# Optimization experiments

Measured on AMD Instinct MI355X. Metric: run time of the kernel, lower is better.

Reference implementation:

```python
import jax, jax.numpy as jnp
import numpy as np

T = 200                      # TRAIN_ROIS_PER_IMAGE
RATIO = 0.33                 # ROI_POSITIVE_RATIO
P_MAX = int(T * RATIO)       # max positive ROIs (66)
MH, MW = 28, 28              # MASK_SHAPE
STD = jnp.array([0.1, 0.1, 0.2, 0.2], jnp.float32)  # BBOX_STD_DEV
EPS = 1e-6


def _iou(a, b):
    # a [N,4], b [G,4] -> [N,G] IoU (same math as overlaps_graph, without tiling)
    ay1, ax1, ay2, ax2 = a[:, 0:1], a[:, 1:2], a[:, 2:3], a[:, 3:4]
    by1, bx1, by2, bx2 = b[None, :, 0], b[None, :, 1], b[None, :, 2], b[None, :, 3]
    iy = jnp.maximum(jnp.minimum(ay2, by2) - jnp.maximum(ay1, by1), 0.0)
    ix = jnp.maximum(jnp.minimum(ax2, bx2) - jnp.maximum(ax1, bx1), 0.0)
    inter = iy * ix
    union = (ay2 - ay1) * (ax2 - ax1) + (by2 - by1) * (bx2 - bx1) - inter
    return inter / jnp.maximum(union, EPS)


def _box_refinement(box, gt):
    # standard Mask R-CNN box_refinement_graph
    h = jnp.maximum(box[:, 2] - box[:, 0], EPS)
    w = jnp.maximum(box[:, 3] - box[:, 1], EPS)
    cy = box[:, 0] + 0.5 * h
    cx = box[:, 1] + 0.5 * w
    gh = jnp.maximum(gt[:, 2] - gt[:, 0], EPS)
    gw = jnp.maximum(gt[:, 3] - gt[:, 1], EPS)
    gcy = gt[:, 0] + 0.5 * gh
    gcx = gt[:, 1] + 0.5 * gw
    return jnp.stack([(gcy - cy) / h, (gcx - cx) / w,
                      jnp.log(gh / h), jnp.log(gw / w)], axis=-1)


def _crop_and_resize(imgs, boxes):
    # imgs [T,H,W], boxes [T,4] normalized; TF crop_and_resize bilinear semantics,
    # extrapolation_value = 0 for samples outside [0, H-1] x [0, W-1].
    Tn, H, W = imgs.shape
    y1, x1, y2, x2 = boxes[:, 0], boxes[:, 1], boxes[:, 2], boxes[:, 3]
    iy = jnp.arange(MH, dtype=jnp.float32)
    ix = jnp.arange(MW, dtype=jnp.float32)
    ys = y1[:, None] * (H - 1) + iy[None, :] * ((y2 - y1) * (H - 1) / (MH - 1))[:, None]  # [T,MH]
    xs = x1[:, None] * (W - 1) + ix[None, :] * ((x2 - x1) * (W - 1) / (MW - 1))[:, None]  # [T,MW]
    y0 = jnp.floor(ys); x0 = jnp.floor(xs)
    wy = (ys - y0)[:, :, None]
    wx = (xs - x0)[:, None, :]
    y0i = jnp.clip(y0, 0, H - 1).astype(jnp.int32)
    y1i = jnp.clip(y0 + 1, 0, H - 1).astype(jnp.int32)
    x0i = jnp.clip(x0, 0, W - 1).astype(jnp.int32)
    x1i = jnp.clip(x0 + 1, 0, W - 1).astype(jnp.int32)
    t = jnp.arange(Tn)[:, None, None]
    v00 = imgs[t, y0i[:, :, None], x0i[:, None, :]]
    v01 = imgs[t, y0i[:, :, None], x1i[:, None, :]]
    v10 = imgs[t, y1i[:, :, None], x0i[:, None, :]]
    v11 = imgs[t, y1i[:, :, None], x1i[:, None, :]]
    val = (v00 * (1 - wx) + v01 * wx) * (1 - wy) + (v10 * (1 - wx) + v11 * wx) * wy
    ok = ((ys >= 0) & (ys <= H - 1))[:, :, None] & ((xs >= 0) & (xs <= W - 1))[:, None, :]
    return jnp.where(ok, val, 0.0)


def _targets_one(proposals, class_ids, boxes, masks):
    # proposals [N,4], class_ids [G] int, boxes [G,4], masks [H,W,G]
    N = proposals.shape[0]
    # zero-padding trim expressed as validity masks (jit-friendly fixed shapes)
    valid_prop = jnp.any(proposals != 0, axis=1)
    valid_gt = jnp.any(boxes != 0, axis=1)
    non_crowd = (class_ids > 0) & valid_gt
    crowd = (class_ids < 0) & valid_gt

    ov = _iou(proposals, boxes)                              # [N,G]
    ov_nc = jnp.where(non_crowd[None, :], ov, -1.0)          # mask crowd/padded gt
    roi_iou_max = ov_nc.max(axis=1)
    crowd_max = jnp.where(crowd[None, :], ov, 0.0).max(axis=1)

    pos_mask = valid_prop & (roi_iou_max >= 0.5)
    neg_mask = valid_prop & (roi_iou_max < 0.5) & (crowd_max < 0.001)

    # deterministic selection (original uses tf.random.shuffle): positives first-in-order
    pos_order = jnp.argsort(jnp.where(pos_mask, 0, 1))
    neg_order = jnp.argsort(jnp.where(neg_mask, 0, 1))
    pos_count = jnp.minimum(pos_mask.sum(), P_MAX)
    neg_needed = jnp.floor(pos_count.astype(jnp.float32) / RATIO).astype(jnp.int32) - pos_count
    neg_count = jnp.minimum(jnp.minimum(neg_needed, neg_mask.sum()), T - pos_count)

    slot = jnp.arange(T)
    is_pos = slot < pos_count
    is_neg = (slot >= pos_count) & (slot < pos_count + neg_count)
    src = jnp.where(is_pos,
                    pos_order[jnp.clip(slot, 0, N - 1)],
                    neg_order[jnp.clip(slot - pos_count, 0, N - 1)])
    rois = jnp.where((is_pos | is_neg)[:, None], proposals[src], 0.0)

    assign = jnp.argmax(ov_nc[src], axis=1)                  # gt assignment per slot
    gt_box = boxes[assign]
    gt_cls = jnp.where(is_pos, class_ids[assign], 0)

    deltas = _box_refinement(rois, gt_box) / STD
    deltas = jnp.where(is_pos[:, None], deltas, 0.0)

    # USE_MINI_MASK: roi box in gt-box-normalized coordinates
    gy1, gx1, gy2, gx2 = gt_box[:, 0], gt_box[:, 1], gt_box[:, 2], gt_box[:, 3]
    gh = jnp.maximum(gy2 - gy1, EPS)
    gw = jnp.maximum(gx2 - gx1, EPS)
    mm = jnp.stack([(rois[:, 0] - gy1) / gh, (rois[:, 1] - gx1) / gw,
                    (rois[:, 2] - gy1) / gh, (rois[:, 3] - gx1) / gw], axis=-1)

    roi_masks = jnp.moveaxis(jnp.take(masks, assign, axis=2), 2, 0)  # [T,H,W]
    m = jnp.round(_crop_and_resize(roi_masks, mm))
    m = jnp.where(is_pos[:, None, None], m, 0.0)
    return rois, gt_cls, deltas, m


def setup_inputs() -> dict:
    key = jax.random.key(0)
    ks = jax.random.split(key, 4)
    B, N, G, HM = 16, 2000, 200, 56

    def boxes_of(k, shape):
        k1, k2, k3, k4 = jax.random.split(k, 4)
        y1 = jax.random.uniform(k1, shape) * 0.5
        x1 = jax.random.uniform(k2, shape) * 0.5
        h = 0.1 + jax.random.uniform(k3, shape) * 0.4
        w = 0.1 + jax.random.uniform(k4, shape) * 0.4
        return jnp.stack([y1, x1, y1 + h, x1 + w], axis=-1)

    proposals = boxes_of(ks[0], (B, N))
    proposals = proposals * (jnp.arange(N) < N - 200)[None, :, None]  # zero-padded tail
    prior_class_ids = jax.random.randint(ks[1], (B, G), -1, 81).astype(jnp.int32)  # -1=crowd, 0=padding
    prior_boxes = boxes_of(ks[2], (B, G)) * (prior_class_ids != 0)[..., None]
    prior_masks = (jax.random.uniform(ks[3], (B, HM, HM, G)) > 0.5).astype(jnp.float32)
    return {"proposals": proposals, "prior_class_ids": prior_class_ids,
            "prior_boxes": prior_boxes, "prior_masks": prior_masks}


def reference(proposals, prior_class_ids, prior_boxes, prior_masks):
    rois, cls, deltas, masks = jax.vmap(_targets_one)(proposals, prior_class_ids,
                                                      prior_boxes, prior_masks)
    return rois, cls, deltas, masks
```

## Files before the change

kernel.cpp:

```cpp
#include <hip/hip_runtime.h>
#include <math.h>

#pragma clang fp contract(off)

#define BN    16
#define NP    2000
#define NG    200
#define NT    200
#define PMAX  66
#define EPSF  1e-6f
#define MH    28
#define MW    28
#define HM    56
#define NPIX  (HM*HM)
#define NW    49
#define NGP   256
#define NPW   32

#define KA_BLOCKS 128
#define KG_BLOCKS (49*4*BN)

__global__ __launch_bounds__(256) void kF(
    const float* __restrict__ proposals, const int* __restrict__ cls_ids,
    const float* __restrict__ boxes, const float* __restrict__ masks,
    unsigned long long* __restrict__ selbits, int* __restrict__ assign_ws,
    unsigned long long* __restrict__ bits)
{
#pragma clang fp contract(off)
  const int tid  = threadIdx.x;
  const int lane = tid & 63;
  const int wv   = tid >> 6;

  __shared__ float4 gbox[NG];
  __shared__ float  garea[NG];
  __shared__ int    gflag[NG];
  __shared__ unsigned long long sw[64];

  if (blockIdx.x < KA_BLOCKS) {
    const int b = blockIdx.x >> 3;
    const int bxa = blockIdx.x & 7;

    for (int j = tid; j < NG; j += 256) {
      float4 g = reinterpret_cast<const float4*>(boxes + (size_t)b * NG * 4)[j];
      int c = cls_ids[b * NG + j];
      bool vg = (g.x != 0.f) || (g.y != 0.f) || (g.z != 0.f) || (g.w != 0.f);
      gbox[j]  = g;
      garea[j] = (g.z - g.x) * (g.w - g.y);
      gflag[j] = vg ? (c > 0 ? 1 : (c < 0 ? 2 : 0)) : 0;
    }
    __syncthreads();

    const int i  = bxa * 256 + tid;
    const bool act = (i < NP);
    const int ic = act ? i : (NP - 1);

    float4 p = reinterpret_cast<const float4*>(proposals + (size_t)b * NP * 4)[ic];
    bool vp = act && ((p.x != 0.f) || (p.y != 0.f) || (p.z != 0.f) || (p.w != 0.f));
    float pa = (p.z - p.x) * (p.w - p.y);

    float best = -3.0e38f;
    int   bestj = 0;
    float cmax = 0.f;
    for (int j = 0; j < NG; ++j) {
      float4 g = gbox[j];
      float iy = fmaxf(fminf(p.z, g.z) - fmaxf(p.x, g.x), 0.f);
      float ix = fmaxf(fminf(p.w, g.w) - fmaxf(p.y, g.y), 0.f);
      float inter = iy * ix;
      float uni = (pa + garea[j]) - inter;
      float iou = inter / fmaxf(uni, EPSF);
      int fl = gflag[j];
      float v = (fl == 1) ? iou : -1.0f;
      if (v > best) { best = v; bestj = j; }
      if (fl == 2) cmax = fmaxf(cmax, iou);
    }
    bool pos = vp && (best >= 0.5f);
    bool neg = vp && (best < 0.5f) && (cmax < 0.001f);
    unsigned long long bp = __ballot(pos);
    unsigned long long bn = __ballot(neg);
    if (lane == 0) {
      int w = bxa * 4 + wv;
      selbits[(size_t)b * 64 + w]       = bp;
      selbits[(size_t)b * 64 + 32 + w]  = bn;
    }
    if (act) assign_ws[b * NP + i] = bestj;
  } else {
    int idx = blockIdx.x - KA_BLOCKS;
    const int pword = idx % 49;
    idx /= 49;
    const int gw0 = (idx & 3) * 64;
    const int b   = idx >> 2;
    const int p0  = pword * 64;

    const bool gok = (gw0 + lane) < NG;
    const float* mbase = masks + (size_t)b * NPIX * NG + gw0 + lane;

    float vv[16];
#pragma unroll
    for (int e = 0; e < 16; ++e) {
      int pl = e * 4 + wv;
      vv[e] = gok ? mbase[(size_t)(p0 + pl) * NG] : 0.f;
    }
#pragma unroll
    for (int e = 0; e < 16; ++e) {
      int pl = e * 4 + wv;
      unsigned long long word = __ballot(vv[e] != 0.f);
      if (lane == 0) sw[pl] = word;
    }
    __syncthreads();

    unsigned long long w0 = sw[lane];
    for (int k = 0; k < 16; ++k) {
      int gl = wv * 16 + k;
      unsigned long long word = __ballot((int)((w0 >> gl) & 1ULL));
      if (lane == 0 && (gw0 + gl) < NG)
        bits[(size_t)(b * NGP + gw0 + gl) * NW + pword] = word;
    }
  }
}

__global__ __launch_bounds__(256) void kB2(
    const float* __restrict__ proposals, const int* __restrict__ cls_ids,
    const float* __restrict__ boxes, const int* __restrict__ assign_ws,
    const unsigned long long* __restrict__ selbits, float* __restrict__ out,
    float* __restrict__ mm_ws, int* __restrict__ ma_ws)
{
#pragma clang fp contract(off)
  const int b = blockIdx.x;
  const int tid = threadIdx.x;

  __shared__ unsigned long long sel[64];
  if (tid < 64) sel[tid] = selbits[(size_t)b * 64 + tid];
  __syncthreads();

  int pos_total = 0, neg_total = 0;
  for (int w = 0; w < NPW; ++w) {
    pos_total += __popcll(sel[w]);
    neg_total += __popcll(sel[32 + w]);
  }
  int pos_count = min(pos_total, PMAX);
  int neg_needed = (int)floorf((float)pos_count / 0.33f) - pos_count;
  int neg_count = min(min(neg_needed, neg_total), NT - pos_count);

  if (tid < NT) {
    const int t = tid;
    const bool ispos = (t < pos_count);
    const bool isneg = (!ispos) && (t < pos_count + neg_count);

    float r0 = 0.f, r1 = 0.f, r2 = 0.f, r3 = 0.f;
    float d0 = 0.f, d1 = 0.f, d2 = 0.f, d3 = 0.f;
    float m0 = 0.f, m1 = 0.f, m2 = 0.f, m3 = 0.f;
    float clsf = 0.f;
    int ma = -1;

    if (ispos || isneg) {
      int k = ispos ? t : (t - pos_count);
      const int base = ispos ? 0 : 32;
      int i = 0;
      for (int w = 0; w < NPW; ++w) {
        unsigned long long word = sel[base + w];
        int c = __popcll(word);
        if (k < c) {
          for (int r = 0; r < k; ++r) word &= word - 1ULL;
          i = w * 64 + __builtin_ctzll(word);
          break;
        }
        k -= c;
      }
      float4 p = reinterpret_cast<const float4*>(proposals + (size_t)b * NP * 4)[i];
      r0 = p.x; r1 = p.y; r2 = p.z; r3 = p.w;
      if (ispos) {
        int a = assign_ws[b * NP + i];
        ma = a;
        float4 g = reinterpret_cast<const float4*>(boxes + (size_t)b * NG * 4)[a];
        float h  = fmaxf(r2 - r0, EPSF);
        float w  = fmaxf(r3 - r1, EPSF);
        float cy = r0 + 0.5f * h;
        float cx = r1 + 0.5f * w;
        float gh = fmaxf(g.z - g.x, EPSF);
        float gw = fmaxf(g.w - g.y, EPSF);
        float gcy = g.x + 0.5f * gh;
        float gcx = g.y + 0.5f * gw;
        d0 = ((gcy - cy) / h) / 0.1f;
        d1 = ((gcx - cx) / w) / 0.1f;
        d2 = logf(gh / h) / 0.2f;
        d3 = logf(gw / w) / 0.2f;
        m0 = (r0 - g.x) / gh;
        m1 = (r1 - g.y) / gw;
        m2 = (r2 - g.x) / gh;
        m3 = (r3 - g.y) / gw;
        clsf = (float)cls_ids[b * NG + a];
      }
    }
    int s = b * NT + tid;
    float* rois = out;
    float* cls  = out + BN * NT * 4;
    float* dlt  = out + BN * NT * 4 + BN * NT;
    rois[s * 4 + 0] = r0; rois[s * 4 + 1] = r1;
    rois[s * 4 + 2] = r2; rois[s * 4 + 3] = r3;
    cls[s] = clsf;
    dlt[s * 4 + 0] = d0; dlt[s * 4 + 1] = d1;
    dlt[s * 4 + 2] = d2; dlt[s * 4 + 3] = d3;
    mm_ws[s * 4 + 0] = m0; mm_ws[s * 4 + 1] = m1;
    mm_ws[s * 4 + 2] = m2; mm_ws[s * 4 + 3] = m3;
    ma_ws[s] = ma;
  }
}

__global__ __launch_bounds__(256) void kC(
    const unsigned long long* __restrict__ bits, const float* __restrict__ mm_ws,
    const int* __restrict__ ma_ws, float* __restrict__ out)
{
#pragma clang fp contract(off)
  const int s = blockIdx.x;
  float4* om = reinterpret_cast<float4*>(
      out + (size_t)(BN * NT * 9) + (size_t)s * (MH * MW));
  const int q = threadIdx.x;
  const int a = ma_ws[s];
  if (a < 0) {
    if (q < (MH * MW) / 4) om[q] = make_float4(0.f, 0.f, 0.f, 0.f);
    return;
  }

  __shared__ unsigned long long pb[NW];
  const int b = s / NT;
  if (q < NW) pb[q] = bits[(size_t)(b * NGP + a) * NW + q];
  __syncthreads();
  if (q >= (MH * MW) / 4) return;

  float y1 = mm_ws[s * 4 + 0], x1 = mm_ws[s * 4 + 1];
  float y2 = mm_ws[s * 4 + 2], x2 = mm_ws[s * 4 + 3];
  float sy = (y2 - y1) * 55.0f / 27.0f;
  float sx = (x2 - x1) * 55.0f / 27.0f;

  int px0 = q * 4;
  int my  = px0 / MW;
  float ys = y1 * 55.0f + (float)my * sy;
  float y0f = floorf(ys);
  float wy  = ys - y0f;
  int y0i = (int)fminf(fmaxf(y0f, 0.f), 55.f);
  int y1i = (int)fminf(fmaxf(y0f + 1.0f, 0.f), 55.f);
  bool oky = (ys >= 0.f) && (ys <= 55.f);
  const int r0b = y0i * HM;
  const int r1b = y1i * HM;

  float res[4];
  for (int k = 0; k < 4; ++k) {
    int mx = (px0 + k) - my * MW;
    float xs = x1 * 55.0f + (float)mx * sx;
    float x0f = floorf(xs);
    float wx  = xs - x0f;
    int x0i = (int)fminf(fmaxf(x0f, 0.f), 55.f);
    int x1i = (int)fminf(fmaxf(x0f + 1.0f, 0.f), 55.f);
    int p00 = r0b + x0i, p01 = r0b + x1i;
    int p10 = r1b + x0i, p11 = r1b + x1i;
    float v00 = (float)((pb[p00 >> 6] >> (p00 & 63)) & 1ULL);
    float v01 = (float)((pb[p01 >> 6] >> (p01 & 63)) & 1ULL);
    float v10 = (float)((pb[p10 >> 6] >> (p10 & 63)) & 1ULL);
    float v11 = (float)((pb[p11 >> 6] >> (p11 & 63)) & 1ULL);
    float val = (v00 * (1.f - wx) + v01 * wx) * (1.f - wy)
              + (v10 * (1.f - wx) + v11 * wx) * wy;
    bool ok = oky && (xs >= 0.f) && (xs <= 55.f);
    res[k] = ok ? rintf(val) : 0.f;
  }
  om[q] = make_float4(res[0], res[1], res[2], res[3]);
}

extern "C" void kernel_launch(void* const* d_in, const int* in_sizes, int n_in,
                              void* d_out, int out_size, void* d_ws, size_t ws_size,
                              hipStream_t stream)
{
  const float* proposals = (const float*)d_in[0];
  const int*   cls_ids   = (const int*)d_in[1];
  const float* boxes     = (const float*)d_in[2];
  const float* masks     = (const float*)d_in[3];
  float* out = (float*)d_out;

  char* ws = (char*)d_ws;
  unsigned long long* selbits = (unsigned long long*)ws;
  ws += (size_t)BN * 64 * sizeof(unsigned long long);
  unsigned long long* bits_ws = (unsigned long long*)ws;
  ws += (size_t)BN * NGP * NW * sizeof(unsigned long long);
  int* assign_ws = (int*)ws;
  ws += (size_t)BN * NP * sizeof(int);
  float* mm_ws = (float*)ws;
  ws += (size_t)BN * NT * 4 * sizeof(float);
  int* ma_ws = (int*)ws;

  kF<<<KA_BLOCKS + KG_BLOCKS, 256, 0, stream>>>(
      proposals, cls_ids, boxes, masks, selbits, assign_ws, bits_ws);
  kB2<<<BN, 256, 0, stream>>>(proposals, cls_ids, boxes, assign_ws, selbits,
                              out, mm_ws, ma_ws);
  kC<<<BN * NT, 256, 0, stream>>>(bits_ws, mm_ws, ma_ws, out);
}
```

Baseline: 114.1 us.

## Load mask rows as float4 and bit-transpose all 200 instances per block

The mask bit-packing branch now lets each block cover all 200 instances for a 64-pixel word. Lanes load float4 vectors along the instance axis and ballot each component, then a transposed ballot writes per-instance words. This cuts the mask-branch block count by four and replaces strided scalar loads with wide, contiguous loads. In exchange, each wave runs a longer serial loop of 50 ballots in the transpose phase, and lanes past 49 repeat lane 49's load.

```diff
diff --git a/kernel.cpp b/kernel.cpp
--- a/kernel.cpp
+++ b/kernel.cpp
@@ -18,7 +18,7 @@
 #define NPW   32
 
 #define KA_BLOCKS 128
-#define KG_BLOCKS (49*4*BN)
+#define KG_BLOCKS (NW*BN)
 
 __global__ __launch_bounds__(256) void kF(
     const float* __restrict__ proposals, const int* __restrict__ cls_ids,
@@ -34,7 +34,7 @@
   __shared__ float4 gbox[NG];
   __shared__ float  garea[NG];
   __shared__ int    gflag[NG];
-  __shared__ unsigned long long sw[64];
+  __shared__ unsigned long long swq[64][4];
 
   if (blockIdx.x < KA_BLOCKS) {
     const int b = blockIdx.x >> 3;
@@ -84,36 +84,40 @@
     }
     if (act) assign_ws[b * NP + i] = bestj;
   } else {
-    int idx = blockIdx.x - KA_BLOCKS;
-    const int pword = idx % 49;
-    idx /= 49;
-    const int gw0 = (idx & 3) * 64;
-    const int b   = idx >> 2;
-    const int p0  = pword * 64;
-
-    const bool gok = (gw0 + lane) < NG;
-    const float* mbase = masks + (size_t)b * NPIX * NG + gw0 + lane;
-
-    float vv[16];
+    const int idx   = blockIdx.x - KA_BLOCKS;
+    const int pword = idx % NW;
+    const int b     = idx / NW;
+    const int p0    = pword * 64;
+
+    const int lc = (lane < 50) ? lane : 49;
+    const float* mb = masks + (size_t)b * NPIX * NG;
+
+    float4 vq[16];
 #pragma unroll
     for (int e = 0; e < 16; ++e) {
-      int pl = e * 4 + wv;
-      vv[e] = gok ? mbase[(size_t)(p0 + pl) * NG] : 0.f;
+      int pl = wv * 16 + e;
+      vq[e] = reinterpret_cast<const float4*>(mb + (size_t)(p0 + pl) * NG)[lc];
     }
 #pragma unroll
     for (int e = 0; e < 16; ++e) {
-      int pl = e * 4 + wv;
-      unsigned long long word = __ballot(vv[e] != 0.f);
-      if (lane == 0) sw[pl] = word;
+      int pl = wv * 16 + e;
+      unsigned long long b0 = __ballot(vq[e].x != 0.f);
+      unsigned long long b1 = __ballot(vq[e].y != 0.f);
+      unsigned long long b2 = __ballot(vq[e].z != 0.f);
+      unsigned long long b3 = __ballot(vq[e].w != 0.f);
+      if (lane == 0) {
+        swq[pl][0] = b0; swq[pl][1] = b1; swq[pl][2] = b2; swq[pl][3] = b3;
+      }
     }
     __syncthreads();
 
-    unsigned long long w0 = sw[lane];
-    for (int k = 0; k < 16; ++k) {
-      int gl = wv * 16 + k;
+    unsigned long long w0 = swq[lane][wv];
+    for (int gl = 0; gl < 50; ++gl) {
       unsigned long long word = __ballot((int)((w0 >> gl) & 1ULL));
-      if (lane == 0 && (gw0 + gl) < NG)
-        bits[(size_t)(b * NGP + gw0 + gl) * NW + pword] = word;
+      if (lane == 0) {
+        int g = 4 * gl + wv;
+        bits[(size_t)(b * NGP + g) * NW + pword] = word;
+      }
     }
   }
 }
```

Measured after the change: 116.5 us. 1.02x slower.
